# Kernel optimization log

Measured on AMD Instinct MI355X. Metric: run time of the kernel, lower is better.

## Reference

```python
import jax, jax.numpy as jnp
import numpy as np

B, S, D, DM, H = 2, 2048, 1024, 1024, 16
DH = D // H
EPS = 1e-5


def layernorm(x, g, b):
    m = jnp.mean(x, axis=-1, keepdims=True)
    v = jnp.mean(jnp.square(x - m), axis=-1, keepdims=True)
    return (x - m) * jax.lax.rsqrt(v + EPS) * g + b


def setup_inputs() -> dict:
    key = jax.random.key(0)
    ks = jax.random.split(key, 16)
    std = 0.02
    p = {
        'x': jax.random.normal(ks[0], (B, S, D), jnp.float32),
        'h': jnp.zeros((B, DM), jnp.float32),
        'c': jnp.zeros((B, DM), jnp.float32),
        'Wq': jax.random.normal(ks[1], (D, D), jnp.float32) * std,
        'Wk': jax.random.normal(ks[2], (D, D), jnp.float32) * std,
        'Wv': jax.random.normal(ks[3], (D, D), jnp.float32) * std,
        'Wo': jax.random.normal(ks[4], (D, D), jnp.float32) * std,
        'Wmk': jax.random.normal(ks[5], (DM, D), jnp.float32) * std,
        'Wmv': jax.random.normal(ks[6], (DM, D), jnp.float32) * std,
        'Wih': jax.random.normal(ks[7], (D, 4 * DM), jnp.float32) * std,
        'Whh': jax.random.normal(ks[8], (DM, 4 * DM), jnp.float32) * std,
        'b_ih': jnp.zeros((4 * DM,), jnp.float32),
        'b_hh': jnp.zeros((4 * DM,), jnp.float32),
        'W1': jax.random.normal(ks[9], (D, 4 * D), jnp.float32) * std,
        'bf1': jnp.zeros((4 * D,), jnp.float32),
        'W2': jax.random.normal(ks[10], (4 * D, D), jnp.float32) * std,
        'bf2': jnp.zeros((D,), jnp.float32),
        'g1': jnp.ones((D,), jnp.float32), 'be1': jnp.zeros((D,), jnp.float32),
        'g2': jnp.ones((D,), jnp.float32), 'be2': jnp.zeros((D,), jnp.float32),
        'g3': jnp.ones((D,), jnp.float32), 'be3': jnp.zeros((D,), jnp.float32),
        'Wmp': jax.random.normal(ks[11], (DM, D), jnp.float32) * std,
    }
    return p


def reference(x, h, c, Wq, Wk, Wv, Wo, Wmk, Wmv, Wih, Whh, b_ih, b_hh,
              W1, bf1, W2, bf2, g1, be1, g2, be2, g3, be3, Wmp):
    xn = layernorm(x, g1, be1)
    # projections, split heads: [B,S,D] -> [B,H,S,DH]
    def heads(t):
        return t.reshape(B, -1, H, DH).transpose(0, 2, 1, 3)
    Q = heads(xn @ Wq)
    Ks = heads(xn @ Wk)
    Vs = heads(xn @ Wv)
    Km = (h @ Wmk).reshape(B, 1, H, DH).transpose(0, 2, 1, 3)  # [B,H,1,DH]
    Vm = (h @ Wmv).reshape(B, 1, H, DH).transpose(0, 2, 1, 3)
    K = jnp.concatenate([Km, Ks], axis=2)  # [B,H,S+1,DH]
    V = jnp.concatenate([Vm, Vs], axis=2)
    scores = jnp.einsum('bhqd,bhkd->bhqk', Q, K) / jnp.sqrt(jnp.float32(DH))
    attn = jax.nn.softmax(scores, axis=-1)
    ao = jnp.einsum('bhqk,bhkd->bhqd', attn, V)
    ao = ao.transpose(0, 2, 1, 3).reshape(B, S, D)
    attended = x + ao @ Wo
    # LSTM step on mean-pooled tokens (torch LSTMCell gate order: i,f,g,o)
    pooled = jnp.mean(attended, axis=1)  # [B,D]
    gates = pooled @ Wih + b_ih + h @ Whh + b_hh
    i, f, g, o = jnp.split(gates, 4, axis=-1)
    new_c = jax.nn.sigmoid(f) * c + jax.nn.sigmoid(i) * jnp.tanh(g)
    new_h = jax.nn.sigmoid(o) * jnp.tanh(new_c)
    mixed = attended + (new_h @ Wmp)[:, None, :]
    hn = layernorm(mixed, g2, be2)
    ffn = jax.nn.gelu(hn @ W1 + bf1, approximate=False) @ W2 + bf2
    out = layernorm(mixed + ffn, g3, be3)
    return (out, new_h, new_c)
```

## Files before the change

kernel.cpp:

```cpp
#include <hip/hip_runtime.h>
#include <hip/hip_bf16.h>
#include <math.h>

#define BB 2
#define SS 2048
#define DD 1024
#define HH 16
#define RR (BB*SS)
#define KSTRIDE 2064
#define MB (1024ull*1024ull)

typedef unsigned short u16;
typedef unsigned int u32;
typedef __attribute__((ext_vector_type(8))) short short8v;
typedef __attribute__((ext_vector_type(4))) float f32x4;
typedef __attribute__((ext_vector_type(16))) float f32x16;
typedef __attribute__((ext_vector_type(4))) u16 u16x4;

__device__ __forceinline__ u16 f2bf(float f){
    union { __hip_bfloat16 h; u16 u; } c; c.h = __float2bfloat16(f); return c.u;
}
__device__ __forceinline__ u32 cvtpk(float a, float b){
    u32 r;
    asm("v_cvt_pk_bf16_f32 %0, %1, %2" : "=v"(r) : "v"(a), "v"(b));
    return r;
}
__device__ __forceinline__ float exp2_raw(float x){
    float r;
    asm("v_exp_f32 %0, %1" : "=v"(r) : "v"(x));
    return r;
}
__device__ __forceinline__ float bf2f(u16 u){
    union { u32 i; float f; } c; c.i = (u32)u << 16; return c.f;
}
__device__ __forceinline__ float erf_fast(float x){
    float ax = fabsf(x);
    float t = __builtin_amdgcn_rcpf(1.0f + 0.3275911f*ax);
    float y = t*(0.254829592f + t*(-0.284496736f + t*(1.421413741f + t*(-1.453152027f + t*1.061405429f))));
    float r = 1.0f - y*__expf(-ax*ax);
    return copysignf(r, x);
}

#define GLL16(gp, lp) __builtin_amdgcn_global_load_lds( \
    (const __attribute__((address_space(1))) void*)(gp), \
    (__attribute__((address_space(3))) void*)(lp), 16, 0, 0)

#define VMCNT8 asm volatile("s_waitcnt vmcnt(8)" ::: "memory")
#define VMCNT4 asm volatile("s_waitcnt vmcnt(4)" ::: "memory")
#define VMCNT0 asm volatile("s_waitcnt vmcnt(0)" ::: "memory")
#define SBAR   __builtin_amdgcn_s_barrier()
#define SCHEDB __builtin_amdgcn_sched_barrier(0)

__global__ __launch_bounds__(256) void ln_kernel(const float* __restrict__ in,
    const float* __restrict__ mproj, const float* __restrict__ g, const float* __restrict__ be,
    float* __restrict__ mixed_out, float* __restrict__ outf, u16* __restrict__ outb)
{
    int row = blockIdx.x; int b = row / SS; int tid = threadIdx.x;
    float4 v = ((const float4*)(in + (size_t)row*DD))[tid];
    if (mproj){
        float4 mp = ((const float4*)(mproj + (size_t)b*DD))[tid];
        v.x+=mp.x; v.y+=mp.y; v.z+=mp.z; v.w+=mp.w;
        ((float4*)(mixed_out + (size_t)row*DD))[tid] = v;
    }
    float s = v.x+v.y+v.z+v.w, s2 = v.x*v.x+v.y*v.y+v.z*v.z+v.w*v.w;
    #pragma unroll
    for (int off=32; off>0; off>>=1){ s += __shfl_down(s,off); s2 += __shfl_down(s2,off); }
    __shared__ float red[2][4];
    if ((tid&63)==0){ red[0][tid>>6]=s; red[1][tid>>6]=s2; }
    __syncthreads();
    float st = red[0][0]+red[0][1]+red[0][2]+red[0][3];
    float s2t= red[1][0]+red[1][1]+red[1][2]+red[1][3];
    float mean = st*(1.f/DD); float var = s2t*(1.f/DD)-mean*mean;
    float rs = rsqrtf(var + 1e-5f);
    float4 gg=((const float4*)g)[tid], bb2=((const float4*)be)[tid];
    float o0=(v.x-mean)*rs*gg.x+bb2.x, o1=(v.y-mean)*rs*gg.y+bb2.y;
    float o2=(v.z-mean)*rs*gg.z+bb2.z, o3=(v.w-mean)*rs*gg.w+bb2.w;
    if (outf){ float4 o={o0,o1,o2,o3}; ((float4*)(outf+(size_t)row*DD))[tid]=o; }
    if (outb){ u16x4 o={f2bf(o0),f2bf(o1),f2bf(o2),f2bf(o3)}; ((u16x4*)(outb+(size_t)row*DD))[tid]=o; }
}

__global__ __launch_bounds__(256) void ln3f_kernel(const u16* __restrict__ pb0,
    const u16* __restrict__ pb1, const u16* __restrict__ pb2, const u16* __restrict__ pb3,
    const float* __restrict__ bias, const float* __restrict__ resid,
    const float* __restrict__ g, const float* __restrict__ be, float* __restrict__ out)
{
    int row = blockIdx.x; int tid = threadIdx.x;
    size_t off = (size_t)row*DD;
    u16x4 q0 = ((const u16x4*)(pb0+off))[tid];
    u16x4 q1 = ((const u16x4*)(pb1+off))[tid];
    u16x4 q2 = ((const u16x4*)(pb2+off))[tid];
    u16x4 q3 = ((const u16x4*)(pb3+off))[tid];
    float4 bi = ((const float4*)bias)[tid];
    float4 rs4= ((const float4*)(resid+off))[tid];
    float4 v;
    v.x = bf2f(q0[0])+bf2f(q1[0])+bf2f(q2[0])+bf2f(q3[0]) + bi.x + rs4.x;
    v.y = bf2f(q0[1])+bf2f(q1[1])+bf2f(q2[1])+bf2f(q3[1]) + bi.y + rs4.y;
    v.z = bf2f(q0[2])+bf2f(q1[2])+bf2f(q2[2])+bf2f(q3[2]) + bi.z + rs4.z;
    v.w = bf2f(q0[3])+bf2f(q1[3])+bf2f(q2[3])+bf2f(q3[3]) + bi.w + rs4.w;
    float s = v.x+v.y+v.z+v.w, s2 = v.x*v.x+v.y*v.y+v.z*v.z+v.w*v.w;
    #pragma unroll
    for (int off2=32; off2>0; off2>>=1){ s += __shfl_down(s,off2); s2 += __shfl_down(s2,off2); }
    __shared__ float red[2][4];
    if ((tid&63)==0){ red[0][tid>>6]=s; red[1][tid>>6]=s2; }
    __syncthreads();
    float st = red[0][0]+red[0][1]+red[0][2]+red[0][3];
    float s2t= red[1][0]+red[1][1]+red[1][2]+red[1][3];
    float mean = st*(1.f/DD); float var = s2t*(1.f/DD)-mean*mean;
    float rs = rsqrtf(var + 1e-5f);
    float4 gg=((const float4*)g)[tid], bb2=((const float4*)be)[tid];
    float4 o;
    o.x=(v.x-mean)*rs*gg.x+bb2.x; o.y=(v.y-mean)*rs*gg.y+bb2.y;
    o.z=(v.z-mean)*rs*gg.z+bb2.z; o.w=(v.w-mean)*rs*gg.w+bb2.w;
    ((float4*)(out + off))[tid] = o;
}

__global__ __launch_bounds__(256) void tr6_kernel(const float* __restrict__ Wq, const float* __restrict__ Wk,
    const float* __restrict__ Wv, const float* __restrict__ Wo,
    const float* __restrict__ W1, const float* __restrict__ W2,
    u16* __restrict__ WqkvT, u16* __restrict__ WoT, u16* __restrict__ W1T, u16* __restrict__ W2T)
{
    __shared__ float t[32][33];
    int bid = blockIdx.x;
    const float* in; u16* out; int K, N, n0, k0;
    if (bid < 3072){
        int m = bid >> 10, r = bid & 1023;
        in = (m==0) ? Wq : (m==1) ? Wk : Wv;
        out = WqkvT + (size_t)m*1024*1024;
        K = 1024; N = 1024; n0 = (r & 31)*32; k0 = (r >> 5)*32;
    } else if (bid < 4096){
        int r = bid - 3072;
        in = Wo; out = WoT; K = 1024; N = 1024; n0 = (r & 31)*32; k0 = (r >> 5)*32;
    } else if (bid < 8192){
        int r = bid - 4096;
        in = W1; out = W1T; K = 1024; N = 4096; n0 = (r & 127)*32; k0 = (r >> 7)*32;
    } else {
        int r = bid - 8192;
        in = W2; out = W2T; K = 4096; N = 1024; n0 = (r & 31)*32; k0 = (r >> 5)*32;
    }
    int tx = threadIdx.x & 31, ty = threadIdx.x >> 5;
    #pragma unroll
    for (int i=0;i<4;i++){ int k = ty + i*8; t[k][tx] = in[(size_t)(k0+k)*N + n0 + tx]; }
    __syncthreads();
    #pragma unroll
    for (int i=0;i<4;i++){ int n = ty + i*8; out[(size_t)(n0+n)*K + k0 + tx] = f2bf(t[tx][n]); }
}

__global__ __launch_bounds__(512) void mgemm256(const u16* __restrict__ A, const u16* __restrict__ BT,
    int nbx, int Kc, int kchunks, int mode, const float* __restrict__ bias, float scale,
    void* __restrict__ Cout, void* __restrict__ C2a, void* __restrict__ C2b, void* __restrict__ C2c)
{
    __shared__ __align__(16) u16 lds[2][2][2][256*32];
    int tid = threadIdx.x, l = tid&63, w = tid>>6;
    int wr = w>>2, wc = w&3;
    int nwg = gridDim.x, q8 = nwg>>3;
    int bid = blockIdx.x;
    int swz = (bid & 7)*q8 + (bid >> 3);
    int tiles = nwg / kchunks;
    int chunk = swz / tiles;
    int t2 = swz % tiles;
    int by = t2 / nbx, bx = t2 % nbx;
    int bm = by*256, bn = bx*256;
    int lda = Kc*kchunks;
    int koff = chunk*Kc;
    const int NT = Kc >> 6;

    f32x4 acc[8][4];
    #pragma unroll
    for (int i=0;i<8;i++)
        #pragma unroll
        for (int j=0;j<4;j++)
            #pragma unroll
            for (int r=0;r<4;r++) acc[i][j][r]=0.f;

    auto stage_plane = [&](int buf, int op, int ks, int tt){
        const u16* base = op ? BT : A;
        int tile0 = op ? bn : bm;
        #pragma unroll
        for (int i=0;i<2;i++){
            int rbase = (w*2+i)*16;
            int row = rbase + (l>>2);
            int slotlog = (l&3) ^ ((row>>1)&3);
            const u16* g = base + (size_t)(tile0 + row)*lda + koff + tt*64 + ks*32 + slotlog*8;
            GLL16(g, (u16*)&lds[buf][op][ks][0] + rbase*32);
        }
    };
    auto ds_a = [&](int buf, int ks, int ai) -> short8v {
        int row = wr*128 + ai*16 + (l&15);
        int slot = (l>>4) ^ ((row>>1)&3);
        return *(const short8v*)((const char*)&lds[buf][0][ks][0] + row*64 + slot*16);
    };
    auto ds_b = [&](int buf, int ks, int bi) -> short8v {
        int row = wc*64 + bi*16 + (l&15);
        int slot = (l>>4) ^ ((row>>1)&3);
        return *(const short8v*)((const char*)&lds[buf][1][ks][0] + row*64 + slot*16);
    };

    stage_plane(0,0,0,0); stage_plane(0,1,0,0);
    stage_plane(0,0,1,0); stage_plane(0,1,1,0);
    stage_plane(1,0,0,1); stage_plane(1,1,0,1);
    VMCNT8;
    SBAR; SCHEDB;

    for (int t=0; t<NT; t++){
        int buf = t&1, obuf = buf^1;
        bool s1 = (t+1 < NT), s2 = (t+2 < NT);
        short8v b0,b1,b2,b3, a0,a1,a2,a3;
        b0=ds_b(buf,0,0); b1=ds_b(buf,0,1); b2=ds_b(buf,0,2); b3=ds_b(buf,0,3);
        a0=ds_a(buf,0,0); a1=ds_a(buf,0,1); a2=ds_a(buf,0,2); a3=ds_a(buf,0,3);
        if (s1) stage_plane(obuf,0,1,t+1);
        __builtin_amdgcn_s_setprio(1);
        acc[0][0]=__builtin_amdgcn_mfma_f32_16x16x32_bf16(b0,a0,acc[0][0],0,0,0);
        acc[0][1]=__builtin_amdgcn_mfma_f32_16x16x32_bf16(b1,a0,acc[0][1],0,0,0);
        acc[0][2]=__builtin_amdgcn_mfma_f32_16x16x32_bf16(b2,a0,acc[0][2],0,0,0);
        acc[0][3]=__builtin_amdgcn_mfma_f32_16x16x32_bf16(b3,a0,acc[0][3],0,0,0);
        acc[1][0]=__builtin_amdgcn_mfma_f32_16x16x32_bf16(b0,a1,acc[1][0],0,0,0);
        acc[1][1]=__builtin_amdgcn_mfma_f32_16x16x32_bf16(b1,a1,acc[1][1],0,0,0);
        acc[1][2]=__builtin_amdgcn_mfma_f32_16x16x32_bf16(b2,a1,acc[1][2],0,0,0);
        acc[1][3]=__builtin_amdgcn_mfma_f32_16x16x32_bf16(b3,a1,acc[1][3],0,0,0);
        acc[2][0]=__builtin_amdgcn_mfma_f32_16x16x32_bf16(b0,a2,acc[2][0],0,0,0);
        acc[2][1]=__builtin_amdgcn_mfma_f32_16x16x32_bf16(b1,a2,acc[2][1],0,0,0);
        acc[2][2]=__builtin_amdgcn_mfma_f32_16x16x32_bf16(b2,a2,acc[2][2],0,0,0);
        acc[2][3]=__builtin_amdgcn_mfma_f32_16x16x32_bf16(b3,a2,acc[2][3],0,0,0);
        acc[3][0]=__builtin_amdgcn_mfma_f32_16x16x32_bf16(b0,a3,acc[3][0],0,0,0);
        acc[3][1]=__builtin_amdgcn_mfma_f32_16x16x32_bf16(b1,a3,acc[3][1],0,0,0);
        acc[3][2]=__builtin_amdgcn_mfma_f32_16x16x32_bf16(b2,a3,acc[3][2],0,0,0);
        acc[3][3]=__builtin_amdgcn_mfma_f32_16x16x32_bf16(b3,a3,acc[3][3],0,0,0);
        __builtin_amdgcn_s_setprio(0);
        SBAR; SCHEDB;
        a0=ds_a(buf,0,4); a1=ds_a(buf,0,5); a2=ds_a(buf,0,6); a3=ds_a(buf,0,7);
        if (s1) stage_plane(obuf,1,1,t+1);
        __builtin_amdgcn_s_setprio(1);
        acc[4][0]=__builtin_amdgcn_mfma_f32_16x16x32_bf16(b0,a0,acc[4][0],0,0,0);
        acc[4][1]=__builtin_amdgcn_mfma_f32_16x16x32_bf16(b1,a0,acc[4][1],0,0,0);
        acc[4][2]=__builtin_amdgcn_mfma_f32_16x16x32_bf16(b2,a0,acc[4][2],0,0,0);
        acc[4][3]=__builtin_amdgcn_mfma_f32_16x16x32_bf16(b3,a0,acc[4][3],0,0,0);
        acc[5][0]=__builtin_amdgcn_mfma_f32_16x16x32_bf16(b0,a1,acc[5][0],0,0,0);
        acc[5][1]=__builtin_amdgcn_mfma_f32_16x16x32_bf16(b1,a1,acc[5][1],0,0,0);
        acc[5][2]=__builtin_amdgcn_mfma_f32_16x16x32_bf16(b2,a1,acc[5][2],0,0,0);
        acc[5][3]=__builtin_amdgcn_mfma_f32_16x16x32_bf16(b3,a1,acc[5][3],0,0,0);
        acc[6][0]=__builtin_amdgcn_mfma_f32_16x16x32_bf16(b0,a2,acc[6][0],0,0,0);
        acc[6][1]=__builtin_amdgcn_mfma_f32_16x16x32_bf16(b1,a2,acc[6][1],0,0,0);
        acc[6][2]=__builtin_amdgcn_mfma_f32_16x16x32_bf16(b2,a2,acc[6][2],0,0,0);
        acc[6][3]=__builtin_amdgcn_mfma_f32_16x16x32_bf16(b3,a2,acc[6][3],0,0,0);
        acc[7][0]=__builtin_amdgcn_mfma_f32_16x16x32_bf16(b0,a3,acc[7][0],0,0,0);
        acc[7][1]=__builtin_amdgcn_mfma_f32_16x16x32_bf16(b1,a3,acc[7][1],0,0,0);
        acc[7][2]=__builtin_amdgcn_mfma_f32_16x16x32_bf16(b2,a3,acc[7][2],0,0,0);
        acc[7][3]=__builtin_amdgcn_mfma_f32_16x16x32_bf16(b3,a3,acc[7][3],0,0,0);
        __builtin_amdgcn_s_setprio(0);
        if (s1) { VMCNT8; } else { VMCNT0; }
        SBAR; SCHEDB;
        b0=ds_b(buf,1,0); b1=ds_b(buf,1,1); b2=ds_b(buf,1,2); b3=ds_b(buf,1,3);
        a0=ds_a(buf,1,0); a1=ds_a(buf,1,1); a2=ds_a(buf,1,2); a3=ds_a(buf,1,3);
        if (s2) stage_plane(buf,0,0,t+2);
        __builtin_amdgcn_s_setprio(1);
        acc[0][0]=__builtin_amdgcn_mfma_f32_16x16x32_bf16(b0,a0,acc[0][0],0,0,0);
        acc[0][1]=__builtin_amdgcn_mfma_f32_16x16x32_bf16(b1,a0,acc[0][1],0,0,0);
        acc[0][2]=__builtin_amdgcn_mfma_f32_16x16x32_bf16(b2,a0,acc[0][2],0,0,0);
        acc[0][3]=__builtin_amdgcn_mfma_f32_16x16x32_bf16(b3,a0,acc[0][3],0,0,0);
        acc[1][0]=__builtin_amdgcn_mfma_f32_16x16x32_bf16(b0,a1,acc[1][0],0,0,0);
        acc[1][1]=__builtin_amdgcn_mfma_f32_16x16x32_bf16(b1,a1,acc[1][1],0,0,0);
        acc[1][2]=__builtin_amdgcn_mfma_f32_16x16x32_bf16(b2,a1,acc[1][2],0,0,0);
        acc[1][3]=__builtin_amdgcn_mfma_f32_16x16x32_bf16(b3,a1,acc[1][3],0,0,0);
        acc[2][0]=__builtin_amdgcn_mfma_f32_16x16x32_bf16(b0,a2,acc[2][0],0,0,0);
        acc[2][1]=__builtin_amdgcn_mfma_f32_16x16x32_bf16(b1,a2,acc[2][1],0,0,0);
        acc[2][2]=__builtin_amdgcn_mfma_f32_16x16x32_bf16(b2,a2,acc[2][2],0,0,0);
        acc[2][3]=__builtin_amdgcn_mfma_f32_16x16x32_bf16(b3,a2,acc[2][3],0,0,0);
        acc[3][0]=__builtin_amdgcn_mfma_f32_16x16x32_bf16(b0,a3,acc[3][0],0,0,0);
        acc[3][1]=__builtin_amdgcn_mfma_f32_16x16x32_bf16(b1,a3,acc[3][1],0,0,0);
        acc[3][2]=__builtin_amdgcn_mfma_f32_16x16x32_bf16(b2,a3,acc[3][2],0,0,0);
        acc[3][3]=__builtin_amdgcn_mfma_f32_16x16x32_bf16(b3,a3,acc[3][3],0,0,0);
        __builtin_amdgcn_s_setprio(0);
        SBAR; SCHEDB;
        a0=ds_a(buf,1,4); a1=ds_a(buf,1,5); a2=ds_a(buf,1,6); a3=ds_a(buf,1,7);
        if (s2) stage_plane(buf,1,0,t+2);
        __builtin_amdgcn_s_setprio(1);
        acc[4][0]=__builtin_amdgcn_mfma_f32_16x16x32_bf16(b0,a0,acc[4][0],0,0,0);
        acc[4][1]=__builtin_amdgcn_mfma_f32_16x16x32_bf16(b1,a0,acc[4][1],0,0,0);
        acc[4][2]=__builtin_amdgcn_mfma_f32_16x16x32_bf16(b2,a0,acc[4][2],0,0,0);
        acc[4][3]=__builtin_amdgcn_mfma_f32_16x16x32_bf16(b3,a0,acc[4][3],0,0,0);
        acc[5][0]=__builtin_amdgcn_mfma_f32_16x16x32_bf16(b0,a1,acc[5][0],0,0,0);
        acc[5][1]=__builtin_amdgcn_mfma_f32_16x16x32_bf16(b1,a1,acc[5][1],0,0,0);
        acc[5][2]=__builtin_amdgcn_mfma_f32_16x16x32_bf16(b2,a1,acc[5][2],0,0,0);
        acc[5][3]=__builtin_amdgcn_mfma_f32_16x16x32_bf16(b3,a1,acc[5][3],0,0,0);
        acc[6][0]=__builtin_amdgcn_mfma_f32_16x16x32_bf16(b0,a2,acc[6][0],0,0,0);
        acc[6][1]=__builtin_amdgcn_mfma_f32_16x16x32_bf16(b1,a2,acc[6][1],0,0,0);
        acc[6][2]=__builtin_amdgcn_mfma_f32_16x16x32_bf16(b2,a2,acc[6][2],0,0,0);
        acc[6][3]=__builtin_amdgcn_mfma_f32_16x16x32_bf16(b3,a2,acc[6][3],0,0,0);
        acc[7][0]=__builtin_amdgcn_mfma_f32_16x16x32_bf16(b0,a3,acc[7][0],0,0,0);
        acc[7][1]=__builtin_amdgcn_mfma_f32_16x16x32_bf16(b1,a3,acc[7][1],0,0,0);
        acc[7][2]=__builtin_amdgcn_mfma_f32_16x16x32_bf16(b2,a3,acc[7][2],0,0,0);
        acc[7][3]=__builtin_amdgcn_mfma_f32_16x16x32_bf16(b3,a3,acc[7][3],0,0,0);
        __builtin_amdgcn_s_setprio(0);
        if (s2) { VMCNT8; } else if (s1) { VMCNT4; } else { VMCNT0; }
        SBAR; SCHEDB;
    }

    int N = nbx*256;
    #pragma unroll
    for (int ai=0; ai<8; ai++){
        int m = bm + wr*128 + ai*16 + (l&15);
        #pragma unroll
        for (int bi=0; bi<4; bi++){
            int nb = bn + wc*64 + bi*16 + ((l>>4)<<2);
            f32x4 v = acc[ai][bi];
            if (mode == 0){
                float4 bv = *(const float4*)(bias + nb);
                float t0=v[0]+bv.x, t1=v[1]+bv.y, t2=v[2]+bv.z, t3=v[3]+bv.w;
                u16x4 o;
                o[0]=f2bf(0.5f*t0*(1.0f+erf_fast(t0*0.70710678118654752f)));
                o[1]=f2bf(0.5f*t1*(1.0f+erf_fast(t1*0.70710678118654752f)));
                o[2]=f2bf(0.5f*t2*(1.0f+erf_fast(t2*0.70710678118654752f)));
                o[3]=f2bf(0.5f*t3*(1.0f+erf_fast(t3*0.70710678118654752f)));
                *(u16x4*)((u16*)Cout + (size_t)m*N + nb) = o;
            } else if (mode == 1){
                if (nb < 1024){
                    u16x4 o;
                    #pragma unroll
                    for (int r=0;r<4;r++) o[r] = f2bf(v[r]*scale);
                    *(u16x4*)((u16*)Cout + (size_t)m*1024 + nb) = o;
                } else if (nb < 2048){
                    int cc = nb-1024; int hh = cc>>6, dh = cc&63;
                    int b2 = m>>11, key = m&2047;
                    u16x4 o;
                    #pragma unroll
                    for (int r=0;r<4;r++) o[r] = f2bf(v[r]);
                    *(u16x4*)((u16*)C2a + ((size_t)(b2*HH+hh)*KSTRIDE + key)*64 + dh) = o;
                } else {
                    int cc = nb-2048; int hh = cc>>6, dh = cc&63;
                    int b2 = m>>11, key = m&2047;
                    #pragma unroll
                    for (int r=0;r<4;r++)
                        ((u16*)C2b)[((size_t)(b2*HH+hh)*64 + dh + r)*KSTRIDE + key] = f2bf(v[r]);
                }
            } else {
                u16* pp = (chunk==0) ? (u16*)Cout : (chunk==1) ? (u16*)C2a :
                          (chunk==2) ? (u16*)C2b : (u16*)C2c;
                u16x4 o;
                #pragma unroll
                for (int r=0;r<4;r++) o[r] = f2bf(v[r]);
                *(u16x4*)(pp + (size_t)m*N + nb) = o;
            }
        }
    }
}

#define MODE_F32R 3

__global__ __launch_bounds__(256) void mgemm(const u16* __restrict__ A, const u16* __restrict__ BT,
    int nbx, int Kc, int kchunks, int mode,
    const float* __restrict__ bias, const float* __restrict__ resid, float scale,
    void* __restrict__ Cout, void* __restrict__ C2a, void* __restrict__ C2b)
{
    int tid=threadIdx.x, l=tid&63, w=tid>>6;
    int nwg = gridDim.x;
    int qq = nwg >> 3;
    int bid = blockIdx.x;
    int swz = (bid & 7)*qq + (bid >> 3);
    int tiles = nwg / kchunks;
    int chunk = swz / tiles;
    int t2 = swz % tiles;
    int sby = t2 / (nbx*8);
    int rem = t2 - sby*(nbx*8);
    int sbx = rem >> 6;
    int ci  = rem & 63;
    int bx = sbx*8 + (ci&7);
    int by = sby*8 + (ci>>3);

    int bm = by*128, bn = bx*128;
    int N = nbx*128;
    int lda = Kc*kchunks;
    int koff = chunk*Kc;
    int wr = w>>1, wc = w&1;
    f32x4 acc[4][4];
    #pragma unroll
    for(int i=0;i<4;i++)
        #pragma unroll
        for(int j=0;j<4;j++)
            #pragma unroll
            for(int r=0;r<4;r++) acc[i][j][r]=0.f;

    __shared__ __align__(16) u16 Al[2][4096];
    __shared__ __align__(16) u16 Bl[2][4096];
    int srow = (w<<4) + (l>>2);
    int sph  = l&3;
    const int NT = Kc >> 5;

    auto stage = [&](int buf, int kt){
        #pragma unroll
        for (int r=0;r<2;r++){
            int rowA = srow + r*64;
            int sl = sph ^ ((rowA>>1)&3);
            const u16* gA = A + (size_t)(bm+rowA)*lda + koff + kt*32 + sl*8;
            GLL16(gA, (char*)&Al[buf][0] + r*4096 + w*1024);
            const u16* gB = BT + (size_t)(bn+rowA)*lda + koff + kt*32 + sl*8;
            GLL16(gB, (char*)&Bl[buf][0] + r*4096 + w*1024);
        }
    };

    int cur=0;
    stage(0,0);
    __syncthreads();
    for (int kt=0; kt<NT; kt++){
        if (kt+1<NT) stage(cur^1, kt+1);
        short8v af[4], bf[4];
        #pragma unroll
        for (int mi=0;mi<4;mi++){
            int row = wr*64 + mi*16 + (l&15);
            int sl = (l>>4) ^ ((row>>1)&3);
            af[mi] = *(const short8v*)((const char*)&Al[cur][0] + row*64 + sl*16);
        }
        #pragma unroll
        for (int ni=0;ni<4;ni++){
            int row = wc*64 + ni*16 + (l&15);
            int sl = (l>>4) ^ ((row>>1)&3);
            bf[ni] = *(const short8v*)((const char*)&Bl[cur][0] + row*64 + sl*16);
        }
        #pragma unroll
        for (int mi=0;mi<4;mi++)
            #pragma unroll
            for (int ni=0;ni<4;ni++)
                acc[mi][ni] = __builtin_amdgcn_mfma_f32_16x16x32_bf16(bf[ni], af[mi], acc[mi][ni], 0,0,0);
        __syncthreads();
        cur ^= 1;
    }

    #pragma unroll
    for (int mi=0;mi<4;mi++){
        int m = bm + wr*64 + mi*16 + (l&15);
        #pragma unroll
        for (int ni=0;ni<4;ni++){
            int nb = bn + wc*64 + ni*16 + ((l>>4)<<2);
            f32x4 v = acc[mi][ni];
            float4 rs = *(const float4*)(resid + (size_t)m*N + nb);
            float4 o = {v[0]+rs.x, v[1]+rs.y, v[2]+rs.z, v[3]+rs.w};
            *(float4*)((float*)Cout + (size_t)m*N + nb) = o;
        }
    }
}

__global__ __launch_bounds__(256) void attn_mfma(const u16* __restrict__ Qb, const u16* __restrict__ Kb,
    const u16* __restrict__ VTb, u16* __restrict__ ao)
{
    __shared__ __align__(16) u16 Kl[3][4096];
    __shared__ __align__(16) u16 Vl[3][4096];
    int tid=threadIdx.x, l=tid&63, w=tid>>6;
    int l31=l&31, hi=l>>5;
    int bid = blockIdx.x;
    int xcd = bid & 7, idx = bid >> 3;
    int bh = xcd*4 + (idx>>4);
    int qt = idx & 15;
    int b=bh>>4, h=bh&15;
    int qrow = qt*128 + w*32 + l31;

    const u16* qptr = Qb + (size_t)(b*SS + qrow)*DD + h*64;
    short8v qf[4];
    #pragma unroll
    for (int t=0;t<4;t++) qf[t] = *(const short8v*)(qptr + t*16 + hi*8);

    f32x16 so0, so1;
    #pragma unroll
    for (int i=0;i<16;i++){ so0[i]=0.f; so1[i]=0.f; }
    float l_run=0.f;

    int skey = (w<<3) + (l>>3);
    int ssl  = l&7;
    auto stage = [&](int buf, int kt){
        #pragma unroll
        for (int r=0;r<2;r++){
            int key = skey + r*32;
            int slot = ssl ^ (key&7);
            const u16* gK = Kb + ((size_t)bh*KSTRIDE + kt*64 + key)*64 + slot*8;
            GLL16(gK, (char*)&Kl[buf][0] + r*4096 + w*1024);
            const u16* gV = VTb + ((size_t)bh*64 + key)*KSTRIDE + kt*64 + slot*8;
            GLL16(gV, (char*)&Vl[buf][0] + r*4096 + w*1024);
        }
    };

    auto QK = [&](int bf, f32x16& s0, f32x16& s1){
        #pragma unroll
        for (int i=0;i<16;i++){ s0[i]=0.f; s1[i]=0.f; }
        __builtin_amdgcn_s_setprio(1);
        #pragma unroll
        for (int t=0;t<4;t++){
            int sl = (2*t+hi) ^ (l31&7);
            short8v kf0 = *(const short8v*)((const char*)&Kl[bf][0] + l31*128 + sl*16);
            s0 = __builtin_amdgcn_mfma_f32_32x32x16_bf16(kf0, qf[t], s0, 0,0,0);
            short8v kf1 = *(const short8v*)((const char*)&Kl[bf][0] + (32+l31)*128 + sl*16);
            s1 = __builtin_amdgcn_mfma_f32_32x32x16_bf16(kf1, qf[t], s1, 0,0,0);
        }
        __builtin_amdgcn_s_setprio(0);
    };

    auto SMPV = [&](int bf, f32x16& s0, f32x16& s1){
        float psum = 0.f;
        #pragma unroll
        for (int r=0;r<16;r++){
            float p=exp2_raw(s0[r]); s0[r]=p; psum+=p;
            float q=exp2_raw(s1[r]); s1[r]=q; psum+=q;
        }
        psum += __shfl_xor(psum, 32);
        l_run += psum;
        short8v pf[4];
        #pragma unroll
        for (int t=0;t<4;t++){
            u32 a0,a1,b0,b1;
            if (t==0){ a0=cvtpk(s0[0],s0[1]);   a1=cvtpk(s0[2],s0[3]);   b0=cvtpk(s0[4],s0[5]);   b1=cvtpk(s0[6],s0[7]); }
            else if (t==1){ a0=cvtpk(s0[8],s0[9]);   a1=cvtpk(s0[10],s0[11]); b0=cvtpk(s0[12],s0[13]); b1=cvtpk(s0[14],s0[15]); }
            else if (t==2){ a0=cvtpk(s1[0],s1[1]);   a1=cvtpk(s1[2],s1[3]);   b0=cvtpk(s1[4],s1[5]);   b1=cvtpk(s1[6],s1[7]); }
            else          { a0=cvtpk(s1[8],s1[9]);   a1=cvtpk(s1[10],s1[11]); b0=cvtpk(s1[12],s1[13]); b1=cvtpk(s1[14],s1[15]); }
            union { u32 u[4]; short8v v; } cvt;
#if __has_builtin(__builtin_amdgcn_permlane32_swap)
            auto r0 = __builtin_amdgcn_permlane32_swap(a0, b0, false, false);
            auto r1 = __builtin_amdgcn_permlane32_swap(a1, b1, false, false);
            cvt.u[0] = (u32)r0[0];
            cvt.u[1] = (u32)r1[0];
            cvt.u[2] = (u32)r0[1];
            cvt.u[3] = (u32)r1[1];
#else
            u32 sx0 = hi ? a0 : b0, sx1 = hi ? a1 : b1;
            u32 r0 = (u32)__shfl_xor((int)sx0, 32);
            u32 r1 = (u32)__shfl_xor((int)sx1, 32);
            cvt.u[0] = hi ? r0 : a0;
            cvt.u[1] = hi ? r1 : a1;
            cvt.u[2] = hi ? b0 : r0;
            cvt.u[3] = hi ? b1 : r1;
#endif
            pf[t] = cvt.v;
        }
        __builtin_amdgcn_s_setprio(1);
        #pragma unroll
        for (int t=0;t<4;t++){
            int sl = (2*t+hi) ^ (l31&7);
            short8v vf0 = *(const short8v*)((const char*)&Vl[bf][0] + l31*128 + sl*16);
            so0 = __builtin_amdgcn_mfma_f32_32x32x16_bf16(vf0, pf[t], so0, 0,0,0);
            short8v vf1 = *(const short8v*)((const char*)&Vl[bf][0] + (32+l31)*128 + sl*16);
            so1 = __builtin_amdgcn_mfma_f32_32x32x16_bf16(vf1, pf[t], so1, 0,0,0);
        }
        __builtin_amdgcn_s_setprio(0);
    };

    const int NTILE = 33;
    int bufA = 0, bufB = 1, bufC = 2;
    stage(0, 0);
    stage(1, 1);
    __syncthreads();

    f32x16 sA0, sA1, sB0, sB1;
    QK(bufA, sA0, sA1);

    auto ITER = [&](f32x16& c0, f32x16& c1, f32x16& n0, f32x16& n1, int t){
        if (t+2 < NTILE) stage(bufC, t+2);
        QK(bufB, n0, n1);
        SMPV(bufA, c0, c1);
        __syncthreads();
        int tmp = bufA; bufA = bufB; bufB = bufC; bufC = tmp;
    };
    #pragma unroll 1
    for (int tt=0; tt<16; tt++){
        ITER(sA0, sA1, sB0, sB1, 2*tt);
        ITER(sB0, sB1, sA0, sA1, 2*tt+1);
    }
    #pragma unroll
    for (int r=0;r<16;r++){
        int k0 = 2048 + (r&3) + 8*(r>>2) + 4*hi;
        if (k0 >= 2049) sA0[r] = -1e30f;
        sA1[r] = -1e30f;
    }
    SMPV(bufA, sA0, sA1);

    float inv = 1.f / l_run;
    u16* aop = ao + (size_t)(b*SS + qrow)*DD + h*64;
    #pragma unroll
    for (int rg=0; rg<4; rg++){
        int dh0 = rg*8 + 4*hi;
        u16x4 o0, o1;
        #pragma unroll
        for (int j=0;j<4;j++){ o0[j]=f2bf(so0[rg*4+j]*inv); o1[j]=f2bf(so1[rg*4+j]*inv); }
        *(u16x4*)(aop + dh0) = o0;
        *(u16x4*)(aop + 32 + dh0) = o1;
    }
}

__global__ __launch_bounds__(256) void vecmat_part(const float* __restrict__ vec,
    const float* __restrict__ W, float* __restrict__ part, int K, int N)
{
    int b = blockIdx.z, kc = blockIdx.y;
    int j = blockIdx.x*256 + threadIdx.x;
    int k0 = kc * (K >> 3);
    float acc = 0.0f;
    #pragma unroll 4
    for (int k = k0; k < k0 + (K >> 3); k++)
        acc += vec[(size_t)b*K + k] * W[(size_t)k*N + j];
    part[((size_t)b*8 + kc)*N + j] = acc;
}

__global__ __launch_bounds__(256) void vecmat_red(const float* __restrict__ part,
    float* __restrict__ out, int N)
{
    int b = blockIdx.y;
    int j = blockIdx.x*256 + threadIdx.x;
    float acc = 0.0f;
    #pragma unroll
    for (int kc = 0; kc < 8; kc++) acc += part[((size_t)b*8 + kc)*N + j];
    out[(size_t)b*N + j] = acc;
}

__global__ __launch_bounds__(256) void vecmat2_part(const float* __restrict__ vec,
    const float* __restrict__ Wa, const float* __restrict__ Wb, float* __restrict__ part)
{
    int b = blockIdx.z, kc = blockIdx.y;
    int j = blockIdx.x*256 + threadIdx.x;
    int k0 = kc * 128;
    float accA = 0.0f, accB = 0.0f;
    #pragma unroll 4
    for (int k = k0; k < k0 + 128; k++){
        float v = vec[(size_t)b*DD + k];
        accA += v * Wa[(size_t)k*DD + j];
        accB += v * Wb[(size_t)k*DD + j];
    }
    part[((size_t)b*8 + kc)*2048 + j] = accA;
    part[((size_t)b*8 + kc)*2048 + 1024 + j] = accB;
}

__global__ __launch_bounds__(256) void vecmat2_red(const float* __restrict__ part,
    float* __restrict__ outA, float* __restrict__ outB)
{
    int b = blockIdx.y;
    int j = blockIdx.x*256 + threadIdx.x;
    float accA = 0.0f, accB = 0.0f;
    #pragma unroll
    for (int kc = 0; kc < 8; kc++){
        accA += part[((size_t)b*8 + kc)*2048 + j];
        accB += part[((size_t)b*8 + kc)*2048 + 1024 + j];
    }
    outA[(size_t)b*DD + j] = accA;
    outB[(size_t)b*DD + j] = accB;
}

__global__ __launch_bounds__(256) void fixup_kernel(const float* __restrict__ Kmb,
    const float* __restrict__ Vmb, u16* __restrict__ Kb, u16* __restrict__ VTb)
{
    int idx = blockIdx.x*256 + threadIdx.x;
    int b = idx>>10, j = idx&1023; int h=j>>6, dh=j&63; int bh=b*HH+h;
    Kb[((size_t)bh*KSTRIDE + 2048)*64 + dh] = f2bf(Kmb[idx]);
    VTb[((size_t)bh*64 + dh)*KSTRIDE + 2048] = f2bf(Vmb[idx]);
}

__global__ __launch_bounds__(256) void pool1_kernel(const float* __restrict__ att, float* __restrict__ ppart)
{
    int b = blockIdx.y, sc = blockIdx.x;
    int tid = threadIdx.x;
    float4 acc = {0,0,0,0};
    for (int s = 0; s < 32; s++) {
        int row = b*SS + sc*32 + s;
        float4 v = ((const float4*)(att + (size_t)row*DD))[tid];
        acc.x += v.x; acc.y += v.y; acc.z += v.z; acc.w += v.w;
    }
    ((float4*)(ppart + ((size_t)b*64 + sc)*DD))[tid] = acc;
}

__global__ __launch_bounds__(256) void pool2_kernel(const float* __restrict__ ppart, float* __restrict__ pooled)
{
    int b = blockIdx.y;
    int j = blockIdx.x*256 + threadIdx.x;
    float acc = 0.0f;
    for (int sc = 0; sc < 64; sc++) acc += ppart[((size_t)b*64 + sc)*DD + j];
    pooled[(size_t)b*DD + j] = acc * (1.0f/SS);
}

__global__ __launch_bounds__(256) void gates_part(const float* __restrict__ pooled,
    const float* __restrict__ h, const float* __restrict__ Wih, const float* __restrict__ Whh,
    float* __restrict__ part)
{
    int b = blockIdx.z, kc = blockIdx.y;
    int j = blockIdx.x*256 + threadIdx.x;
    int k0 = kc * 64;
    float acc = 0.0f;
    #pragma unroll 4
    for (int k = k0; k < k0 + 64; k++)
        acc += pooled[(size_t)b*DD + k] * Wih[(size_t)k*4*DD + j]
             + h[(size_t)b*DD + k]      * Whh[(size_t)k*4*DD + j];
    part[((size_t)b*16 + kc)*4*DD + j] = acc;
}

__device__ __forceinline__ float sigmoidf_(float x) { return 1.0f / (1.0f + __expf(-x)); }

__global__ __launch_bounds__(256) void lstm_kernel(const float* __restrict__ gpart,
    const float* __restrict__ b_ih, const float* __restrict__ b_hh,
    const float* __restrict__ c, float* __restrict__ newh_ws, float* __restrict__ out_tail)
{
    int idx = blockIdx.x*256 + threadIdx.x;
    int b = idx >> 10, d = idx & 1023;
    float sI = b_ih[d]          + b_hh[d];
    float sF = b_ih[DD + d]     + b_hh[DD + d];
    float sG = b_ih[2*DD + d]   + b_hh[2*DD + d];
    float sO = b_ih[3*DD + d]   + b_hh[3*DD + d];
    #pragma unroll
    for (int kc = 0; kc < 16; kc++){
        const float* gp = gpart + ((size_t)b*16 + kc)*4*DD;
        sI += gp[d]; sF += gp[DD + d]; sG += gp[2*DD + d]; sO += gp[3*DD + d];
    }
    float ig = sigmoidf_(sI);
    float fg = sigmoidf_(sF);
    float gg = tanhf(sG);
    float og = sigmoidf_(sO);
    float nc = fg * c[idx] + ig * gg;
    float nh = og * tanhf(nc);
    newh_ws[idx] = nh;
    out_tail[idx] = nh;
    out_tail[BB*DD + idx] = nc;
}

extern "C" void kernel_launch(void* const* d_in, const int* in_sizes, int n_in,
                              void* d_out, int out_size, void* d_ws, size_t ws_size,
                              hipStream_t stream) {
    const float* x    = (const float*)d_in[0];
    const float* h    = (const float*)d_in[1];
    const float* c    = (const float*)d_in[2];
    const float* Wq   = (const float*)d_in[3];
    const float* Wk   = (const float*)d_in[4];
    const float* Wv   = (const float*)d_in[5];
    const float* Wo   = (const float*)d_in[6];
    const float* Wmk  = (const float*)d_in[7];
    const float* Wmv  = (const float*)d_in[8];
    const float* Wih  = (const float*)d_in[9];
    const float* Whh  = (const float*)d_in[10];
    const float* b_ih = (const float*)d_in[11];
    const float* b_hh = (const float*)d_in[12];
    const float* W1   = (const float*)d_in[13];
    const float* bf1  = (const float*)d_in[14];
    const float* W2   = (const float*)d_in[15];
    const float* bf2  = (const float*)d_in[16];
    const float* g1   = (const float*)d_in[17];
    const float* be1  = (const float*)d_in[18];
    const float* g2   = (const float*)d_in[19];
    const float* be2  = (const float*)d_in[20];
    const float* g3   = (const float*)d_in[21];
    const float* be3  = (const float*)d_in[22];
    const float* Wmp  = (const float*)d_in[23];

    float* out = (float*)d_out;
    char* wsb  = (char*)d_ws;

    u16*   xn   = (u16*)(wsb + 0);
    u16*   hn   = (u16*)(wsb + 8*MB);
    u16*   pb0  = (u16*)(wsb + 0);
    u16*   pb1  = (u16*)(wsb + 8*MB);
    u16*   Qbuf = (u16*)(wsb + 16*MB);
    u16*   Kbuf = (u16*)(wsb + 24*MB);
    u16*   VTb  = (u16*)(wsb + 33*MB);
    u16*   act  = (u16*)(wsb + 16*MB);
    u16*   ao   = (u16*)(wsb + 48*MB);
    u16*   pb2  = (u16*)(wsb + 48*MB);
    float* attb = (float*)(wsb + 56*MB);
    u16*   WqkvT= (u16*)(wsb + 72*MB);
    u16*   WoT  = (u16*)(wsb + 78*MB);
    u16*   W1T  = (u16*)(wsb + 80*MB);
    u16*   pb3  = (u16*)(wsb + 80*MB);
    u16*   W2T  = (u16*)(wsb + 88*MB);
    float* sm   = (float*)(wsb + 96*MB);
    float* Kmb     = sm;
    float* Vmb     = Kmb + 2048;
    float* pooled  = Vmb + 2048;
    float* newh    = pooled + 2048;
    float* mproj   = newh + 2048;
    float* vpart   = mproj + 2048;
    float* v2part  = vpart + 16384;
    float* gpart   = v2part + 32768;
    float* ppart   = gpart + 131072;

    tr6_kernel<<<12288, 256, 0, stream>>>(Wq, Wk, Wv, Wo, W1, W2, WqkvT, WoT, W1T, W2T);

    ln_kernel<<<RR, 256, 0, stream>>>(x, nullptr, g1, be1, nullptr, nullptr, xn);
    vecmat2_part<<<dim3(4,8,BB), 256, 0, stream>>>(h, Wmk, Wmv, v2part);
    vecmat2_red<<<dim3(4,BB), 256, 0, stream>>>(v2part, Kmb, Vmb);
    mgemm256<<<192, 512, 0, stream>>>(xn, WqkvT, 12, 1024, 1, 1, nullptr,
                                      0.125f*1.44269504088896f, Qbuf, Kbuf, VTb, nullptr);
    fixup_kernel<<<8, 256, 0, stream>>>(Kmb, Vmb, Kbuf, VTb);
    attn_mfma<<<512, 256, 0, stream>>>(Qbuf, Kbuf, VTb, ao);
    mgemm<<<8*32, 256, 0, stream>>>(ao, WoT, 8, 1024, 1, MODE_F32R, nullptr, x, 1.f, attb, nullptr, nullptr);
    pool1_kernel<<<dim3(64,BB), 256, 0, stream>>>(attb, ppart);
    pool2_kernel<<<dim3(4,BB), 256, 0, stream>>>(ppart, pooled);
    gates_part<<<dim3(16,16,BB), 256, 0, stream>>>(pooled, h, Wih, Whh, gpart);
    lstm_kernel<<<8, 256, 0, stream>>>(gpart, b_ih, b_hh, c, newh, out + (size_t)RR*DD);
    vecmat_part<<<dim3(4,8,BB), 256, 0, stream>>>(newh, Wmp, vpart, DD, DD);
    vecmat_red<<<dim3(4,BB), 256, 0, stream>>>(vpart, mproj, DD);
    ln_kernel<<<RR, 256, 0, stream>>>(attb, mproj, g2, be2, attb, nullptr, hn);
    mgemm256<<<256, 512, 0, stream>>>(hn, W1T, 16, 1024, 1, 0, bf1, 1.f, act, nullptr, nullptr, nullptr);
    mgemm256<<<256, 512, 0, stream>>>(act, W2T, 4, 1024, 4, 2, nullptr, 1.f, pb0, pb1, pb2, pb3);
    ln3f_kernel<<<RR, 256, 0, stream>>>(pb0, pb1, pb2, pb3, bf2, attb, g3, be3, out);
}
```

Before: 291.0 us.

## Give each wave private 32-key KV buffers and drop block-wide barriers in attention

The attention kernel stops sharing 64-key K/V tiles across the block with triple buffering and __syncthreads. Each wave now loads its own 32-key K and V tiles into a private double-buffered LDS region and waits on vmcnt instead of a block barrier. This is meant to remove block-wide synchronisation stalls and let waves run independently. In exchange, every wave loads the same K/V data, so global/L2 traffic for K/V rises about fourfold. The loop also runs twice as many iterations with smaller MFMA batches, and the QK of the next tile no longer overlaps the softmax of the current one.

```diff
diff --git a/kernel.cpp b/kernel.cpp
--- a/kernel.cpp
+++ b/kernel.cpp
@@ -441,8 +441,7 @@
 __global__ __launch_bounds__(256) void attn_mfma(const u16* __restrict__ Qb, const u16* __restrict__ Kb,
     const u16* __restrict__ VTb, u16* __restrict__ ao)
 {
-    __shared__ __align__(16) u16 Kl[3][4096];
-    __shared__ __align__(16) u16 Vl[3][4096];
+    __shared__ __align__(16) u16 KV[4][2][2][2048];
     int tid=threadIdx.x, l=tid&63, w=tid>>6;
     int l31=l&31, hi=l>>5;
     int bid = blockIdx.x;
@@ -462,52 +461,59 @@
     for (int i=0;i<16;i++){ so0[i]=0.f; so1[i]=0.f; }
     float l_run=0.f;
 
-    int skey = (w<<3) + (l>>3);
-    int ssl  = l&7;
     auto stage = [&](int buf, int kt){
         #pragma unroll
-        for (int r=0;r<2;r++){
-            int key = skey + r*32;
-            int slot = ssl ^ (key&7);
-            const u16* gK = Kb + ((size_t)bh*KSTRIDE + kt*64 + key)*64 + slot*8;
-            GLL16(gK, (char*)&Kl[buf][0] + r*4096 + w*1024);
-            const u16* gV = VTb + ((size_t)bh*64 + key)*KSTRIDE + kt*64 + slot*8;
-            GLL16(gV, (char*)&Vl[buf][0] + r*4096 + w*1024);
+        for (int i=0;i<4;i++){
+            int row = i*8 + (l>>3);
+            int slot = (l&7) ^ (row&7);
+            const u16* gK = Kb + ((size_t)bh*KSTRIDE + kt*32 + row)*64 + slot*8;
+            GLL16(gK, (u16*)&KV[w][buf][0][0] + i*512);
+        }
+        #pragma unroll
+        for (int i=0;i<4;i++){
+            int row = i*16 + (l>>2);
+            int slot = (l&3) ^ (row&3);
+            const u16* gV = VTb + ((size_t)bh*64 + row)*KSTRIDE + kt*32 + slot*8;
+            GLL16(gV, (u16*)&KV[w][buf][1][0] + i*512);
         }
     };
 
-    auto QK = [&](int bf, f32x16& s0, f32x16& s1){
-        #pragma unroll
-        for (int i=0;i<16;i++){ s0[i]=0.f; s1[i]=0.f; }
+    stage(0, 0);
+    const int NT32 = 65;
+    #pragma unroll 1
+    for (int t=0; t<NT32; t++){
+        int buf = t&1;
+        if (t+1 < NT32){ stage(buf^1, t+1); VMCNT8; } else { VMCNT0; }
+        SCHEDB;
+        f32x16 ss;
+        #pragma unroll
+        for (int i=0;i<16;i++) ss[i]=0.f;
         __builtin_amdgcn_s_setprio(1);
         #pragma unroll
-        for (int t=0;t<4;t++){
-            int sl = (2*t+hi) ^ (l31&7);
-            short8v kf0 = *(const short8v*)((const char*)&Kl[bf][0] + l31*128 + sl*16);
-            s0 = __builtin_amdgcn_mfma_f32_32x32x16_bf16(kf0, qf[t], s0, 0,0,0);
-            short8v kf1 = *(const short8v*)((const char*)&Kl[bf][0] + (32+l31)*128 + sl*16);
-            s1 = __builtin_amdgcn_mfma_f32_32x32x16_bf16(kf1, qf[t], s1, 0,0,0);
+        for (int tt=0;tt<4;tt++){
+            int sl = (2*tt+hi) ^ (l31&7);
+            short8v kf = *(const short8v*)((const char*)&KV[w][buf][0][0] + l31*128 + sl*16);
+            ss = __builtin_amdgcn_mfma_f32_32x32x16_bf16(kf, qf[tt], ss, 0,0,0);
         }
         __builtin_amdgcn_s_setprio(0);
-    };
-
-    auto SMPV = [&](int bf, f32x16& s0, f32x16& s1){
+        if (t == NT32-1){
+            #pragma unroll
+            for (int r=0;r<16;r++){
+                int k0 = 2048 + (r&3) + 8*(r>>2) + 4*hi;
+                if (k0 >= 2049) ss[r] = -1e30f;
+            }
+        }
         float psum = 0.f;
         #pragma unroll
-        for (int r=0;r<16;r++){
-            float p=exp2_raw(s0[r]); s0[r]=p; psum+=p;
-            float q=exp2_raw(s1[r]); s1[r]=q; psum+=q;
-        }
+        for (int r=0;r<16;r++){ float p=exp2_raw(ss[r]); ss[r]=p; psum+=p; }
         psum += __shfl_xor(psum, 32);
         l_run += psum;
-        short8v pf[4];
-        #pragma unroll
-        for (int t=0;t<4;t++){
+        short8v pf[2];
+        #pragma unroll
+        for (int tt=0;tt<2;tt++){
             u32 a0,a1,b0,b1;
-            if (t==0){ a0=cvtpk(s0[0],s0[1]);   a1=cvtpk(s0[2],s0[3]);   b0=cvtpk(s0[4],s0[5]);   b1=cvtpk(s0[6],s0[7]); }
-            else if (t==1){ a0=cvtpk(s0[8],s0[9]);   a1=cvtpk(s0[10],s0[11]); b0=cvtpk(s0[12],s0[13]); b1=cvtpk(s0[14],s0[15]); }
-            else if (t==2){ a0=cvtpk(s1[0],s1[1]);   a1=cvtpk(s1[2],s1[3]);   b0=cvtpk(s1[4],s1[5]);   b1=cvtpk(s1[6],s1[7]); }
-            else          { a0=cvtpk(s1[8],s1[9]);   a1=cvtpk(s1[10],s1[11]); b0=cvtpk(s1[12],s1[13]); b1=cvtpk(s1[14],s1[15]); }
+            if (tt==0){ a0=cvtpk(ss[0],ss[1]);  a1=cvtpk(ss[2],ss[3]);   b0=cvtpk(ss[4],ss[5]);   b1=cvtpk(ss[6],ss[7]); }
+            else      { a0=cvtpk(ss[8],ss[9]);  a1=cvtpk(ss[10],ss[11]); b0=cvtpk(ss[12],ss[13]); b1=cvtpk(ss[14],ss[15]); }
             union { u32 u[4]; short8v v; } cvt;
 #if __has_builtin(__builtin_amdgcn_permlane32_swap)
             auto r0 = __builtin_amdgcn_permlane32_swap(a0, b0, false, false);
@@ -525,48 +531,19 @@
             cvt.u[2] = hi ? b0 : r0;
             cvt.u[3] = hi ? b1 : r1;
 #endif
-            pf[t] = cvt.v;
+            pf[tt] = cvt.v;
         }
         __builtin_amdgcn_s_setprio(1);
         #pragma unroll
-        for (int t=0;t<4;t++){
-            int sl = (2*t+hi) ^ (l31&7);
-            short8v vf0 = *(const short8v*)((const char*)&Vl[bf][0] + l31*128 + sl*16);
-            so0 = __builtin_amdgcn_mfma_f32_32x32x16_bf16(vf0, pf[t], so0, 0,0,0);
-            short8v vf1 = *(const short8v*)((const char*)&Vl[bf][0] + (32+l31)*128 + sl*16);
-            so1 = __builtin_amdgcn_mfma_f32_32x32x16_bf16(vf1, pf[t], so1, 0,0,0);
+        for (int tt=0;tt<2;tt++){
+            int sl = (2*tt+hi) ^ (l31&3);
+            short8v vf0 = *(const short8v*)((const char*)&KV[w][buf][1][0] + l31*64 + sl*16);
+            so0 = __builtin_amdgcn_mfma_f32_32x32x16_bf16(vf0, pf[tt], so0, 0,0,0);
+            short8v vf1 = *(const short8v*)((const char*)&KV[w][buf][1][0] + (32+l31)*64 + sl*16);
+            so1 = __builtin_amdgcn_mfma_f32_32x32x16_bf16(vf1, pf[tt], so1, 0,0,0);
         }
         __builtin_amdgcn_s_setprio(0);
-    };
-
-    const int NTILE = 33;
-    int bufA = 0, bufB = 1, bufC = 2;
-    stage(0, 0);
-    stage(1, 1);
-    __syncthreads();
-
-    f32x16 sA0, sA1, sB0, sB1;
-    QK(bufA, sA0, sA1);
-
-    auto ITER = [&](f32x16& c0, f32x16& c1, f32x16& n0, f32x16& n1, int t){
-        if (t+2 < NTILE) stage(bufC, t+2);
-        QK(bufB, n0, n1);
-        SMPV(bufA, c0, c1);
-        __syncthreads();
-        int tmp = bufA; bufA = bufB; bufB = bufC; bufC = tmp;
-    };
-    #pragma unroll 1
-    for (int tt=0; tt<16; tt++){
-        ITER(sA0, sA1, sB0, sB1, 2*tt);
-        ITER(sB0, sB1, sA0, sA1, 2*tt+1);
-    }
-    #pragma unroll
-    for (int r=0;r<16;r++){
-        int k0 = 2048 + (r&3) + 8*(r>>2) + 4*hi;
-        if (k0 >= 2049) sA0[r] = -1e30f;
-        sA1[r] = -1e30f;
-    }
-    SMPV(bufA, sA0, sA1);
+    }
 
     float inv = 1.f / l_run;
     u16* aop = ao + (size_t)(b*SS + qrow)*DD + h*64;
```

Measured after the change: 298.8 us. 2.7% more time.
